# Kernel optimization log

Hardware: AMD Instinct MI355X
Metric: run time of the kernel (lower is better)

Reference implementation:

```python
import jax, jax.numpy as jnp
import numpy as np

ALPHA = 0.2  # LeakyReLU negative slope
NEG = -9e15


def _gat_heads(x, adj_mask, W, a):
    # x: (B,N,F); W: (H,F,O); a: (H,2O); adj_mask: (B,N,N) bool
    O = W.shape[-1]
    Wh = jnp.einsum('bnf,hfo->bhno', x, W)            # (B,H,N,O)
    e1 = jnp.einsum('bhno,ho->bhn', Wh, a[:, :O])     # Wh @ a[:O]
    e2 = jnp.einsum('bhno,ho->bhn', Wh, a[:, O:])     # Wh @ a[O:]
    e = jax.nn.leaky_relu(e1[:, :, :, None] + e2[:, :, None, :], ALPHA)  # (B,H,N,N)
    e = jnp.where(adj_mask[:, None], e, NEG)
    attn = jax.nn.softmax(e, axis=-1)
    return jnp.einsum('bhnm,bhmo->bhno', attn, Wh)    # (B,H,N,O)


def _gat_block(x, adj_mask, non_pad_mask, W_heads, a_heads, W_out, a_out):
    # multi-head layer, concat=True -> elu per head, then concat on feature dim
    h = jax.nn.elu(_gat_heads(x, adj_mask, W_heads, a_heads))  # (B,H,N,O)
    B, H, N, O = h.shape
    h = jnp.transpose(h, (0, 2, 1, 3)).reshape(B, N, H * O)
    h = h * non_pad_mask
    # out layer: single head, concat=False (no inner elu)
    h = _gat_heads(h, adj_mask, W_out[None], a_out[None])[:, 0]  # (B,N,noutput)
    h = h * non_pad_mask
    return jax.nn.elu(h)


def setup_inputs() -> dict:
    key = jax.random.key(0)
    ks = jax.random.split(key, 8)
    B, N = 32, 256
    vocab, F, O, H, OUT = 200, 300, 256, 8, 512
    fea = jax.random.randint(ks[0], (B, N), 0, vocab, dtype=jnp.int32)
    adj = jax.random.randint(ks[1], (B, N, N), 0, 2, dtype=jnp.int32)
    non_pad_mask = jnp.ones((B, N, 1), dtype=jnp.float32)
    embed = jax.random.normal(ks[2], (vocab, F), dtype=jnp.float32)
    W_heads = jax.random.normal(ks[3], (H, F, O), dtype=jnp.float32) / np.sqrt(F)
    a_heads = jax.random.normal(ks[4], (H, 2 * O), dtype=jnp.float32) / np.sqrt(2 * O)
    W_out = jax.random.normal(ks[5], (H * O, OUT), dtype=jnp.float32) / np.sqrt(H * O)
    a_out = jax.random.normal(ks[6], (2 * OUT,), dtype=jnp.float32) / np.sqrt(2 * OUT)
    return {"fea": fea, "adj": adj, "non_pad_mask": non_pad_mask, "embed": embed,
            "W_heads": W_heads, "a_heads": a_heads, "W_out": W_out, "a_out": a_out}


def reference(fea, adj, non_pad_mask, embed, W_heads, a_heads, W_out, a_out):
    adj_mask = adj > 0
    x = embed[fea]  # (B,N,F)
    # GAT_num = 1; dropout is identity in eval mode
    x = _gat_block(x, adj_mask, non_pad_mask, W_heads, a_heads, W_out, a_out)
    return x  # (B, N, 512)
```

## Files before the change

### kernel.cpp

```cpp
#include <hip/hip_runtime.h>
#include <math.h>


typedef _Float16 f16;
typedef __attribute__((ext_vector_type(8))) _Float16 f16x8;
typedef __attribute__((ext_vector_type(4))) _Float16 f16x4;
typedef __attribute__((ext_vector_type(4))) float f32x4;

__device__ __forceinline__ void async16(const void* g, void* lds) {
  __builtin_amdgcn_global_load_lds(
      (const __attribute__((address_space(1))) void*)g,
      (__attribute__((address_space(3))) void*)lds, 16, 0, 0);
}

__global__ __launch_bounds__(256) void k_prep(const int* __restrict__ fea,
                                              const float* __restrict__ embed,
                                              const float* __restrict__ Whd,
                                              const float* __restrict__ Wo,
                                              f16* __restrict__ x16,
                                              f16* __restrict__ WcT,
                                              f16* __restrict__ WoT,
                                              float* __restrict__ e_all) {
  int bid = blockIdx.x, tid = threadIdx.x;
  if (bid < 1280) {
    int idx = bid * 256 + tid;
    int row = idx / 40, c = idx % 40;
    int tok = fea[row];
    const float* eb = embed + (size_t)tok * 300;
    f16x8 v;
#pragma unroll
    for (int j = 0; j < 8; ++j) {
      int t = c * 8 + j;
      v[j] = (f16)((t < 300) ? eb[t] : 0.f);
    }
    *(f16x8*)&x16[(size_t)row * 320 + c * 8] = v;
  } else if (bid < 1920) {
    int r = bid - 1280;
    int zi = r * 256 + tid;
    if (zi < 147456) e_all[zi] = 0.f;
    __shared__ float tile[32][33];
    int bx = r % 10, q0 = r / 10;
    int by = q0 % 8, h = q0 / 8;
    int c = tid & 31, q = tid >> 5;
#pragma unroll
    for (int i = 0; i < 4; ++i) {
      int tt = q + i * 8;
      int t = bx * 32 + tt;
      float v = (t < 300) ? Whd[((size_t)h * 300 + t) * 256 + by * 32 + c] : 0.f;
      tile[tt][c] = v;
    }
    __syncthreads();
#pragma unroll
    for (int i = 0; i < 4; ++i) {
      int oo = q + i * 8;
      int gc = h * 256 + by * 32 + oo;
      WcT[(size_t)gc * 320 + bx * 32 + c] = (f16)tile[c][oo];
    }
  } else {
    int r = bid - 1920;
    __shared__ float tile[32][33];
    int bx = r % 64, by = r / 64;
    int c = tid & 31, q = tid >> 5;
#pragma unroll
    for (int i = 0; i < 4; ++i) {
      int kk = q + i * 8;
      tile[kk][c] = Wo[((size_t)bx * 32 + kk) * 512 + by * 32 + c];
    }
    __syncthreads();
#pragma unroll
    for (int i = 0; i < 4; ++i) {
      int oo = q + i * 8;
      WoT[((size_t)by * 32 + oo) * 2048 + bx * 32 + c] = (f16)tile[c][oo];
    }
  }
}

template <int KDIM, int NCOLS>
__global__ __launch_bounds__(256, 4) void k_gemm1(const f16* __restrict__ A,
                                                  const f16* __restrict__ BT,
                                                  f16* __restrict__ outT,
                                                  const float* __restrict__ avec,
                                                  float* __restrict__ e1,
                                                  float* __restrict__ e2) {
  __shared__ f16 As[128 * 64];
  __shared__ f16 Bs[128 * 64];
  const int by = blockIdx.x, bx = blockIdx.y;
  const int tid = threadIdx.x;
  const int wave = tid >> 6, lane = tid & 63;
  const int wm = wave >> 1, wn = wave & 1;
  const int lrow = lane & 15, quad = lane >> 4;
  const int srow = lane >> 3;
  const int scol = ((lane & 7) ^ (lane >> 3)) * 8;
  const int l7 = lrow & 7;

  f32x4 acc[4][4] = {};
  const f16* Ag = A + (size_t)by * 128 * KDIM;
  const f16* Bg = BT + (size_t)bx * 128 * KDIM;

  for (int k0 = 0; k0 < KDIM; k0 += 64) {
    __syncthreads();
#pragma unroll
    for (int j = 0; j < 4; ++j) {
      const int r0 = wave * 32 + j * 8;
      async16(Ag + (size_t)(r0 + srow) * KDIM + k0 + scol, &As[r0 * 64]);
      async16(Bg + (size_t)(r0 + srow) * KDIM + k0 + scol, &Bs[r0 * 64]);
    }
    __syncthreads();
#pragma unroll
    for (int s = 0; s < 2; ++s) {
      const int sq = ((s * 4 + quad) ^ l7) * 8;
      f16x8 af[4], bf[4];
#pragma unroll
      for (int t = 0; t < 4; ++t) {
        af[t] = *(const f16x8*)&As[(wm * 64 + t * 16 + lrow) * 64 + sq];
        bf[t] = *(const f16x8*)&Bs[(wn * 64 + t * 16 + lrow) * 64 + sq];
      }
#pragma unroll
      for (int mt = 0; mt < 4; ++mt)
#pragma unroll
        for (int nt = 0; nt < 4; ++nt)
          acc[mt][nt] = __builtin_amdgcn_mfma_f32_16x16x32_f16(af[mt], bf[nt], acc[mt][nt], 0, 0, 0);
    }
  }

  const int b = (by * 128) >> 8;
  const int nbase0 = (by * 128) & 255;
#pragma unroll
  for (int mt = 0; mt < 4; ++mt) {
    const int nb = nbase0 + wm * 64 + mt * 16 + quad * 4;
#pragma unroll
    for (int nt = 0; nt < 4; ++nt) {
      const int gc = bx * 128 + wn * 64 + nt * 16 + lrow;
      f16x4 v;
#pragma unroll
      for (int r = 0; r < 4; ++r) v[r] = (f16)acc[mt][nt][r];
      *(f16x4*)&outT[((size_t)b * NCOLS + gc) * 256 + nb] = v;
    }
  }

  float a1v[4], a2v[4];
#pragma unroll
  for (int nt = 0; nt < 4; ++nt) {
    const int gc = bx * 128 + wn * 64 + nt * 16 + lrow;
    int hh = gc >> 8, oo = gc & 255;
    a1v[nt] = avec[hh * 512 + oo];
    a2v[nt] = avec[hh * 512 + 256 + oo];
  }
  const int hblk = (bx * 128) >> 8;
  const int ebase = (b * 8 + hblk) * 256;
#pragma unroll
  for (int mt = 0; mt < 4; ++mt) {
    float s1[4] = {0.f, 0.f, 0.f, 0.f}, s2[4] = {0.f, 0.f, 0.f, 0.f};
#pragma unroll
    for (int nt = 0; nt < 4; ++nt)
#pragma unroll
      for (int r = 0; r < 4; ++r) {
        s1[r] += acc[mt][nt][r] * a1v[nt];
        s2[r] += acc[mt][nt][r] * a2v[nt];
      }
#pragma unroll
    for (int r = 0; r < 4; ++r)
#pragma unroll
      for (int m = 1; m < 16; m <<= 1) {
        s1[r] += __shfl_xor(s1[r], m);
        s2[r] += __shfl_xor(s2[r], m);
      }
    if (lrow == 0) {
      const int nb = nbase0 + wm * 64 + mt * 16 + quad * 4;
#pragma unroll
      for (int r = 0; r < 4; ++r) {
        atomicAdd(&e1[ebase + nb + r], s1[r]);
        atomicAdd(&e2[ebase + nb + r], s2[r]);
      }
    }
  }
}

__global__ __launch_bounds__(256, 4) void k_gemm_sk(const f16* __restrict__ A,
                                                    const f16* __restrict__ BT,
                                                    f16* __restrict__ outSK,
                                                    const float* __restrict__ ao,
                                                    float* __restrict__ e12,
                                                    float* __restrict__ e22) {
  __shared__ f16 As[128 * 64];
  __shared__ f16 Bs[64 * 64];
  const int by = blockIdx.x, bx = blockIdx.y, kz = blockIdx.z;
  const int tid = threadIdx.x;
  const int wave = tid >> 6, lane = tid & 63;
  const int wm = wave >> 1, wn = wave & 1;
  const int lrow = lane & 15, quad = lane >> 4;
  const int srow = lane >> 3;
  const int scol = ((lane & 7) ^ (lane >> 3)) * 8;
  const int l7 = lrow & 7;

  f32x4 acc[4][2] = {};
  const f16* Ag = A + (size_t)by * 128 * 2048;
  const f16* Bg = BT + (size_t)bx * 64 * 2048;
  const int kbeg = kz * 1024;

  for (int k0 = kbeg; k0 < kbeg + 1024; k0 += 64) {
    __syncthreads();
#pragma unroll
    for (int j = 0; j < 4; ++j) {
      const int r0 = wave * 32 + j * 8;
      async16(Ag + (size_t)(r0 + srow) * 2048 + k0 + scol, &As[r0 * 64]);
    }
#pragma unroll
    for (int j = 0; j < 2; ++j) {
      const int r0 = wave * 16 + j * 8;
      async16(Bg + (size_t)(r0 + srow) * 2048 + k0 + scol, &Bs[r0 * 64]);
    }
    __syncthreads();
#pragma unroll
    for (int s = 0; s < 2; ++s) {
      const int sq = ((s * 4 + quad) ^ l7) * 8;
      f16x8 af[4], bf[2];
#pragma unroll
      for (int t = 0; t < 4; ++t)
        af[t] = *(const f16x8*)&As[(wm * 64 + t * 16 + lrow) * 64 + sq];
#pragma unroll
      for (int t = 0; t < 2; ++t)
        bf[t] = *(const f16x8*)&Bs[(wn * 32 + t * 16 + lrow) * 64 + sq];
#pragma unroll
      for (int mt = 0; mt < 4; ++mt)
#pragma unroll
        for (int nt = 0; nt < 2; ++nt)
          acc[mt][nt] = __builtin_amdgcn_mfma_f32_16x16x32_f16(af[mt], bf[nt], acc[mt][nt], 0, 0, 0);
    }
  }

  const int b = (by * 128) >> 8;
  const int nbase0 = (by * 128) & 255;
  f16* dst = outSK + (size_t)kz * 32 * 512 * 256;
#pragma unroll
  for (int mt = 0; mt < 4; ++mt) {
    const int nb = nbase0 + wm * 64 + mt * 16 + quad * 4;
#pragma unroll
    for (int nt = 0; nt < 2; ++nt) {
      const int gc = bx * 64 + wn * 32 + nt * 16 + lrow;
      f16x4 v;
#pragma unroll
      for (int r = 0; r < 4; ++r) v[r] = (f16)acc[mt][nt][r];
      *(f16x4*)&dst[((size_t)b * 512 + gc) * 256 + nb] = v;
    }
  }

  float a1v[2], a2v[2];
#pragma unroll
  for (int nt = 0; nt < 2; ++nt) {
    const int gc = bx * 64 + wn * 32 + nt * 16 + lrow;
    a1v[nt] = ao[gc];
    a2v[nt] = ao[512 + gc];
  }
#pragma unroll
  for (int mt = 0; mt < 4; ++mt) {
    float s1[4] = {0.f, 0.f, 0.f, 0.f}, s2[4] = {0.f, 0.f, 0.f, 0.f};
#pragma unroll
    for (int nt = 0; nt < 2; ++nt)
#pragma unroll
      for (int r = 0; r < 4; ++r) {
        s1[r] += acc[mt][nt][r] * a1v[nt];
        s2[r] += acc[mt][nt][r] * a2v[nt];
      }
#pragma unroll
    for (int r = 0; r < 4; ++r)
#pragma unroll
      for (int m = 1; m < 16; m <<= 1) {
        s1[r] += __shfl_xor(s1[r], m);
        s2[r] += __shfl_xor(s2[r], m);
      }
    if (lrow == 0) {
      const int nb = nbase0 + wm * 64 + mt * 16 + quad * 4;
#pragma unroll
      for (int r = 0; r < 4; ++r) {
        atomicAdd(&e12[b * 256 + nb + r], s1[r]);
        atomicAdd(&e22[b * 256 + nb + r], s2[r]);
      }
    }
  }
}

#define PSTRIDE 264

__global__ __launch_bounds__(256, 4) void k_attn1(
    const f16* __restrict__ WhT, const float* __restrict__ e1g, const float* __restrict__ e2g,
    const int* __restrict__ adj, const float* __restrict__ npm, f16* __restrict__ h1) {
  int h = blockIdx.x, b = blockIdx.y, nt0 = blockIdx.z;
  int bh = b * 8 + h;
  int n0 = nt0 * 64;
  __shared__ f16 P[64 * PSTRIDE];
  int tid = threadIdx.x;
  int wave = tid >> 6, lane = tid & 63;

  float4 e2v = *(const float4*)&e2g[bh * 256 + lane * 4];
  float e2m = fmaxf(fmaxf(e2v.x, e2v.y), fmaxf(e2v.z, e2v.w));
#pragma unroll
  for (int m = 1; m < 64; m <<= 1) e2m = fmaxf(e2m, __shfl_xor(e2m, m));
#pragma unroll 4
  for (int i = 0; i < 16; ++i) {
    int row = i * 4 + wave;
    int gn = b * 256 + n0 + row;
    float er = e1g[bh * 256 + n0 + row];
    float sh = er + e2m;
    sh = sh > 0.f ? sh : 0.2f * sh;
    int4 aj = *(const int4*)&adj[(size_t)gn * 256 + lane * 4];
    float p0, p1, p2, p3;
    {
      float v = er + e2v.x; v = v > 0.f ? v : 0.2f * v;
      p0 = aj.x ? __expf(v - sh) : 0.f;
      v = er + e2v.y; v = v > 0.f ? v : 0.2f * v;
      p1 = aj.y ? __expf(v - sh) : 0.f;
      v = er + e2v.z; v = v > 0.f ? v : 0.2f * v;
      p2 = aj.z ? __expf(v - sh) : 0.f;
      v = er + e2v.w; v = v > 0.f ? v : 0.2f * v;
      p3 = aj.w ? __expf(v - sh) : 0.f;
    }
    float sm = p0 + p1 + p2 + p3;
#pragma unroll
    for (int m = 1; m < 64; m <<= 1) sm += __shfl_xor(sm, m);
    float rs = 1.f / sm;
    f16x4 pw;
    pw[0] = (f16)(p0 * rs); pw[1] = (f16)(p1 * rs);
    pw[2] = (f16)(p2 * rs); pw[3] = (f16)(p3 * rs);
    *(f16x4*)&P[row * PSTRIDE + lane * 4] = pw;
  }
  __syncthreads();

  int lrow = lane & 15, quad = lane >> 4;
  f32x4 acc[4][4] = {};
  const f16* Ag = WhT + (size_t)bh * 65536;
#pragma unroll 2
  for (int k0 = 0; k0 < 256; k0 += 32) {
    f16x8 af[4], bf[4];
#pragma unroll
    for (int mt = 0; mt < 4; ++mt)
      af[mt] = *(const f16x8*)&Ag[(size_t)(wave * 64 + mt * 16 + lrow) * 256 + k0 + quad * 8];
#pragma unroll
    for (int nt = 0; nt < 4; ++nt)
      bf[nt] = *(const f16x8*)&P[(nt * 16 + lrow) * PSTRIDE + k0 + quad * 8];
#pragma unroll
    for (int mt = 0; mt < 4; ++mt)
#pragma unroll
      for (int nt = 0; nt < 4; ++nt)
        acc[mt][nt] = __builtin_amdgcn_mfma_f32_16x16x32_f16(af[mt], bf[nt], acc[mt][nt], 0, 0, 0);
  }
#pragma unroll
  for (int nt = 0; nt < 4; ++nt) {
    int nloc = nt * 16 + lrow;
    int gn = b * 256 + n0 + nloc;
    float pm = npm[gn];
#pragma unroll
    for (int mt = 0; mt < 4; ++mt) {
      int o0 = wave * 64 + mt * 16 + quad * 4;
      f16x4 st;
#pragma unroll
      for (int r = 0; r < 4; ++r) {
        float v = acc[mt][nt][r];
        v = v > 0.f ? v : (__expf(v) - 1.f);
        st[r] = (f16)(v * pm);
      }
      *(f16x4*)&h1[(size_t)gn * 2048 + h * 256 + o0] = st;
    }
  }
}

__global__ __launch_bounds__(256, 4) void k_attn2(
    const f16* __restrict__ sk, const float* __restrict__ e1g, const float* __restrict__ e2g,
    const int* __restrict__ adj, const float* __restrict__ npm, float* __restrict__ out) {
  int oh = blockIdx.x, b = blockIdx.y, nt0 = blockIdx.z;
  int n0 = nt0 * 64;
  __shared__ f16 P[64 * PSTRIDE];
  int tid = threadIdx.x;
  int wave = tid >> 6, lane = tid & 63;

  float4 e2v = *(const float4*)&e2g[b * 256 + lane * 4];
  float e2m = fmaxf(fmaxf(e2v.x, e2v.y), fmaxf(e2v.z, e2v.w));
#pragma unroll
  for (int m = 1; m < 64; m <<= 1) e2m = fmaxf(e2m, __shfl_xor(e2m, m));
#pragma unroll 4
  for (int i = 0; i < 16; ++i) {
    int row = i * 4 + wave;
    int gn = b * 256 + n0 + row;
    float er = e1g[b * 256 + n0 + row];
    float sh = er + e2m;
    sh = sh > 0.f ? sh : 0.2f * sh;
    int4 aj = *(const int4*)&adj[(size_t)gn * 256 + lane * 4];
    float p0, p1, p2, p3;
    {
      float v = er + e2v.x; v = v > 0.f ? v : 0.2f * v;
      p0 = aj.x ? __expf(v - sh) : 0.f;
      v = er + e2v.y; v = v > 0.f ? v : 0.2f * v;
      p1 = aj.y ? __expf(v - sh) : 0.f;
      v = er + e2v.z; v = v > 0.f ? v : 0.2f * v;
      p2 = aj.z ? __expf(v - sh) : 0.f;
      v = er + e2v.w; v = v > 0.f ? v : 0.2f * v;
      p3 = aj.w ? __expf(v - sh) : 0.f;
    }
    float sm = p0 + p1 + p2 + p3;
#pragma unroll
    for (int m = 1; m < 64; m <<= 1) sm += __shfl_xor(sm, m);
    float rs = 1.f / sm;
    f16x4 pw;
    pw[0] = (f16)(p0 * rs); pw[1] = (f16)(p1 * rs);
    pw[2] = (f16)(p2 * rs); pw[3] = (f16)(p3 * rs);
    *(f16x4*)&P[row * PSTRIDE + lane * 4] = pw;
  }
  __syncthreads();

  int lrow = lane & 15, quad = lane >> 4;
  f32x4 acc[2][4] = {};
  const f16* Ag0 = sk + ((size_t)b * 512 + oh * 128) * 256;
  const f16* Ag1 = Ag0 + (size_t)32 * 512 * 256;
#pragma unroll 2
  for (int k0 = 0; k0 < 256; k0 += 32) {
    f16x8 af[2], bf[4];
#pragma unroll
    for (int mt = 0; mt < 2; ++mt) {
      size_t off = (size_t)(wave * 32 + mt * 16 + lrow) * 256 + k0 + quad * 8;
      af[mt] = *(const f16x8*)&Ag0[off] + *(const f16x8*)&Ag1[off];
    }
#pragma unroll
    for (int nt = 0; nt < 4; ++nt)
      bf[nt] = *(const f16x8*)&P[(nt * 16 + lrow) * PSTRIDE + k0 + quad * 8];
#pragma unroll
    for (int mt = 0; mt < 2; ++mt)
#pragma unroll
      for (int nt = 0; nt < 4; ++nt)
        acc[mt][nt] = __builtin_amdgcn_mfma_f32_16x16x32_f16(af[mt], bf[nt], acc[mt][nt], 0, 0, 0);
  }
#pragma unroll
  for (int nt = 0; nt < 4; ++nt) {
    int nloc = nt * 16 + lrow;
    int gn = b * 256 + n0 + nloc;
    float pm = npm[gn];
#pragma unroll
    for (int mt = 0; mt < 2; ++mt) {
      int o0 = oh * 128 + wave * 32 + mt * 16 + quad * 4;
      float4 st;
      float v0 = acc[mt][nt][0] * pm;
      float v1 = acc[mt][nt][1] * pm;
      float v2 = acc[mt][nt][2] * pm;
      float v3 = acc[mt][nt][3] * pm;
      st.x = v0 > 0.f ? v0 : (__expf(v0) - 1.f);
      st.y = v1 > 0.f ? v1 : (__expf(v1) - 1.f);
      st.z = v2 > 0.f ? v2 : (__expf(v2) - 1.f);
      st.w = v3 > 0.f ? v3 : (__expf(v3) - 1.f);
      *(float4*)&out[(size_t)gn * 512 + o0] = st;
    }
  }
}

extern "C" void kernel_launch(void* const* d_in, const int* in_sizes, int n_in,
                              void* d_out, int out_size, void* d_ws, size_t ws_size,
                              hipStream_t stream) {
  (void)in_sizes; (void)n_in; (void)out_size; (void)ws_size;
  const int*   fea   = (const int*)d_in[0];
  const int*   adj   = (const int*)d_in[1];
  const float* npm   = (const float*)d_in[2];
  const float* embed = (const float*)d_in[3];
  const float* Whd   = (const float*)d_in[4];
  const float* ah    = (const float*)d_in[5];
  const float* Wo    = (const float*)d_in[6];
  const float* ao    = (const float*)d_in[7];
  float* out = (float*)d_out;

  char* ws = (char*)d_ws;
  f16* x16  = (f16*)ws;  ws += (size_t)8192 * 320 * 2;
  f16* WcT  = (f16*)ws;  ws += (size_t)2048 * 320 * 2;
  f16* WoT  = (f16*)ws;  ws += (size_t)512 * 2048 * 2;
  f16* WhT  = (f16*)ws;  ws += (size_t)32 * 8 * 256 * 256 * 2;
  f16* h1   = (f16*)ws;  ws += (size_t)8192 * 2048 * 2;
  f16* Wh2sk = (f16*)ws; ws += (size_t)2 * 32 * 512 * 256 * 2;
  float* e1  = (float*)ws; ws += (size_t)65536 * 4;
  float* e2  = (float*)ws; ws += (size_t)65536 * 4;
  float* e12 = (float*)ws; ws += (size_t)8192 * 4;
  float* e22 = (float*)ws; ws += (size_t)8192 * 4;

  k_prep<<<2944, 256, 0, stream>>>(fea, embed, Whd, Wo, x16, WcT, WoT, e1);

  k_gemm1<320, 2048><<<dim3(64, 16), 256, 0, stream>>>(x16, WcT, WhT, ah, e1, e2);
  k_attn1<<<dim3(8, 32, 4), 256, 0, stream>>>(WhT, e1, e2, adj, npm, h1);

  k_gemm_sk<<<dim3(64, 8, 2), 256, 0, stream>>>(h1, WoT, Wh2sk, ao, e12, e22);
  k_attn2<<<dim3(4, 32, 4), 256, 0, stream>>>(Wh2sk, e12, e22, adj, npm, out);
}
```

Measured before the change: 201.9 us.

## Double-buffer LDS tiles in GEMMs and software-prefetch global operands in attention

Both projection GEMMs now use two LDS buffers, issuing async global-to-LDS loads for the next K tile while MFMAs consume the current one, with one barrier per iteration instead of two. Launch-bound occupancy hints drop to 2 and 3 blocks per CU to fit the doubled shared memory. Both attention kernels now ping-pong register fragments, loading the next K slice of Wh from global memory before issuing MFMAs on the current one. This aims to hide memory latency, at the cost of lower occupancy and more register pressure.

```diff
diff --git a/kernel.cpp b/kernel.cpp
--- a/kernel.cpp
+++ b/kernel.cpp
@@ -76,14 +76,14 @@
 }
 
 template <int KDIM, int NCOLS>
-__global__ __launch_bounds__(256, 4) void k_gemm1(const f16* __restrict__ A,
+__global__ __launch_bounds__(256, 2) void k_gemm1(const f16* __restrict__ A,
                                                   const f16* __restrict__ BT,
                                                   f16* __restrict__ outT,
                                                   const float* __restrict__ avec,
                                                   float* __restrict__ e1,
                                                   float* __restrict__ e2) {
-  __shared__ f16 As[128 * 64];
-  __shared__ f16 Bs[128 * 64];
+  __shared__ f16 As[2][128 * 64];
+  __shared__ f16 Bs[2][128 * 64];
   const int by = blockIdx.x, bx = blockIdx.y;
   const int tid = threadIdx.x;
   const int wave = tid >> 6, lane = tid & 63;
@@ -96,24 +96,36 @@
   f32x4 acc[4][4] = {};
   const f16* Ag = A + (size_t)by * 128 * KDIM;
   const f16* Bg = BT + (size_t)bx * 128 * KDIM;
-
-  for (int k0 = 0; k0 < KDIM; k0 += 64) {
-    __syncthreads();
-#pragma unroll
-    for (int j = 0; j < 4; ++j) {
-      const int r0 = wave * 32 + j * 8;
-      async16(Ag + (size_t)(r0 + srow) * KDIM + k0 + scol, &As[r0 * 64]);
-      async16(Bg + (size_t)(r0 + srow) * KDIM + k0 + scol, &Bs[r0 * 64]);
-    }
-    __syncthreads();
+  constexpr int NT = KDIM / 64;
+
+#pragma unroll
+  for (int j = 0; j < 4; ++j) {
+    const int r0 = wave * 32 + j * 8;
+    async16(Ag + (size_t)(r0 + srow) * KDIM + scol, &As[0][r0 * 64]);
+    async16(Bg + (size_t)(r0 + srow) * KDIM + scol, &Bs[0][r0 * 64]);
+  }
+  __syncthreads();
+
+#pragma unroll
+  for (int t = 0; t < NT; ++t) {
+    const int cur = t & 1;
+    if (t + 1 < NT) {
+      const int kn = (t + 1) * 64;
+#pragma unroll
+      for (int j = 0; j < 4; ++j) {
+        const int r0 = wave * 32 + j * 8;
+        async16(Ag + (size_t)(r0 + srow) * KDIM + kn + scol, &As[cur ^ 1][r0 * 64]);
+        async16(Bg + (size_t)(r0 + srow) * KDIM + kn + scol, &Bs[cur ^ 1][r0 * 64]);
+      }
+    }
 #pragma unroll
     for (int s = 0; s < 2; ++s) {
       const int sq = ((s * 4 + quad) ^ l7) * 8;
       f16x8 af[4], bf[4];
 #pragma unroll
-      for (int t = 0; t < 4; ++t) {
-        af[t] = *(const f16x8*)&As[(wm * 64 + t * 16 + lrow) * 64 + sq];
-        bf[t] = *(const f16x8*)&Bs[(wn * 64 + t * 16 + lrow) * 64 + sq];
+      for (int tt = 0; tt < 4; ++tt) {
+        af[tt] = *(const f16x8*)&As[cur][(wm * 64 + tt * 16 + lrow) * 64 + sq];
+        bf[tt] = *(const f16x8*)&Bs[cur][(wn * 64 + tt * 16 + lrow) * 64 + sq];
       }
 #pragma unroll
       for (int mt = 0; mt < 4; ++mt)
@@ -121,6 +133,7 @@
         for (int nt = 0; nt < 4; ++nt)
           acc[mt][nt] = __builtin_amdgcn_mfma_f32_16x16x32_f16(af[mt], bf[nt], acc[mt][nt], 0, 0, 0);
     }
+    __syncthreads();
   }
 
   const int b = (by * 128) >> 8;
@@ -176,14 +189,14 @@
   }
 }
 
-__global__ __launch_bounds__(256, 4) void k_gemm_sk(const f16* __restrict__ A,
+__global__ __launch_bounds__(256, 3) void k_gemm_sk(const f16* __restrict__ A,
                                                     const f16* __restrict__ BT,
                                                     f16* __restrict__ outSK,
                                                     const float* __restrict__ ao,
                                                     float* __restrict__ e12,
                                                     float* __restrict__ e22) {
-  __shared__ f16 As[128 * 64];
-  __shared__ f16 Bs[64 * 64];
+  __shared__ f16 As[2][128 * 64];
+  __shared__ f16 Bs[2][64 * 64];
   const int by = blockIdx.x, bx = blockIdx.y, kz = blockIdx.z;
   const int tid = threadIdx.x;
   const int wave = tid >> 6, lane = tid & 63;
@@ -198,35 +211,51 @@
   const f16* Bg = BT + (size_t)bx * 64 * 2048;
   const int kbeg = kz * 1024;
 
-  for (int k0 = kbeg; k0 < kbeg + 1024; k0 += 64) {
-    __syncthreads();
-#pragma unroll
-    for (int j = 0; j < 4; ++j) {
-      const int r0 = wave * 32 + j * 8;
-      async16(Ag + (size_t)(r0 + srow) * 2048 + k0 + scol, &As[r0 * 64]);
-    }
-#pragma unroll
-    for (int j = 0; j < 2; ++j) {
-      const int r0 = wave * 16 + j * 8;
-      async16(Bg + (size_t)(r0 + srow) * 2048 + k0 + scol, &Bs[r0 * 64]);
-    }
-    __syncthreads();
+#pragma unroll
+  for (int j = 0; j < 4; ++j) {
+    const int r0 = wave * 32 + j * 8;
+    async16(Ag + (size_t)(r0 + srow) * 2048 + kbeg + scol, &As[0][r0 * 64]);
+  }
+#pragma unroll
+  for (int j = 0; j < 2; ++j) {
+    const int r0 = wave * 16 + j * 8;
+    async16(Bg + (size_t)(r0 + srow) * 2048 + kbeg + scol, &Bs[0][r0 * 64]);
+  }
+  __syncthreads();
+
+#pragma unroll 2
+  for (int t = 0; t < 16; ++t) {
+    const int cur = t & 1;
+    if (t + 1 < 16) {
+      const int kn = kbeg + (t + 1) * 64;
+#pragma unroll
+      for (int j = 0; j < 4; ++j) {
+        const int r0 = wave * 32 + j * 8;
+        async16(Ag + (size_t)(r0 + srow) * 2048 + kn + scol, &As[cur ^ 1][r0 * 64]);
+      }
+#pragma unroll
+      for (int j = 0; j < 2; ++j) {
+        const int r0 = wave * 16 + j * 8;
+        async16(Bg + (size_t)(r0 + srow) * 2048 + kn + scol, &Bs[cur ^ 1][r0 * 64]);
+      }
+    }
 #pragma unroll
     for (int s = 0; s < 2; ++s) {
       const int sq = ((s * 4 + quad) ^ l7) * 8;
       f16x8 af[4], bf[2];
 #pragma unroll
-      for (int t = 0; t < 4; ++t)
-        af[t] = *(const f16x8*)&As[(wm * 64 + t * 16 + lrow) * 64 + sq];
-#pragma unroll
-      for (int t = 0; t < 2; ++t)
-        bf[t] = *(const f16x8*)&Bs[(wn * 32 + t * 16 + lrow) * 64 + sq];
+      for (int tt = 0; tt < 4; ++tt)
+        af[tt] = *(const f16x8*)&As[cur][(wm * 64 + tt * 16 + lrow) * 64 + sq];
+#pragma unroll
+      for (int tt = 0; tt < 2; ++tt)
+        bf[tt] = *(const f16x8*)&Bs[cur][(wn * 32 + tt * 16 + lrow) * 64 + sq];
 #pragma unroll
       for (int mt = 0; mt < 4; ++mt)
 #pragma unroll
         for (int nt = 0; nt < 2; ++nt)
           acc[mt][nt] = __builtin_amdgcn_mfma_f32_16x16x32_f16(af[mt], bf[nt], acc[mt][nt], 0, 0, 0);
     }
+    __syncthreads();
   }
 
   const int b = (by * 128) >> 8;
@@ -281,6 +310,13 @@
 }
 
 #define PSTRIDE 264
+
+__device__ __forceinline__ void load_af4(const f16* __restrict__ Ag, int wave,
+                                         int lrow, int quad, int k0, f16x8* dst) {
+#pragma unroll
+  for (int mt = 0; mt < 4; ++mt)
+    dst[mt] = *(const f16x8*)&Ag[(size_t)(wave * 64 + mt * 16 + lrow) * 256 + k0 + quad * 8];
+}
 
 __global__ __launch_bounds__(256, 4) void k_attn1(
     const f16* __restrict__ WhT, const float* __restrict__ e1g, const float* __restrict__ e2g,
@@ -329,12 +365,13 @@
   int lrow = lane & 15, quad = lane >> 4;
   f32x4 acc[4][4] = {};
   const f16* Ag = WhT + (size_t)bh * 65536;
-#pragma unroll 2
-  for (int k0 = 0; k0 < 256; k0 += 32) {
-    f16x8 af[4], bf[4];
-#pragma unroll
-    for (int mt = 0; mt < 4; ++mt)
-      af[mt] = *(const f16x8*)&Ag[(size_t)(wave * 64 + mt * 16 + lrow) * 256 + k0 + quad * 8];
+  f16x8 afA[4], afB[4];
+  load_af4(Ag, wave, lrow, quad, 0, afA);
+#pragma unroll
+  for (int kk = 0; kk < 4; ++kk) {
+    const int k0 = kk * 64;
+    load_af4(Ag, wave, lrow, quad, k0 + 32, afB);
+    f16x8 bf[4];
 #pragma unroll
     for (int nt = 0; nt < 4; ++nt)
       bf[nt] = *(const f16x8*)&P[(nt * 16 + lrow) * PSTRIDE + k0 + quad * 8];
@@ -342,7 +379,16 @@
     for (int mt = 0; mt < 4; ++mt)
 #pragma unroll
       for (int nt = 0; nt < 4; ++nt)
-        acc[mt][nt] = __builtin_amdgcn_mfma_f32_16x16x32_f16(af[mt], bf[nt], acc[mt][nt], 0, 0, 0);
+        acc[mt][nt] = __builtin_amdgcn_mfma_f32_16x16x32_f16(afA[mt], bf[nt], acc[mt][nt], 0, 0, 0);
+    if (kk < 3) load_af4(Ag, wave, lrow, quad, k0 + 64, afA);
+#pragma unroll
+    for (int nt = 0; nt < 4; ++nt)
+      bf[nt] = *(const f16x8*)&P[(nt * 16 + lrow) * PSTRIDE + k0 + 32 + quad * 8];
+#pragma unroll
+    for (int mt = 0; mt < 4; ++mt)
+#pragma unroll
+      for (int nt = 0; nt < 4; ++nt)
+        acc[mt][nt] = __builtin_amdgcn_mfma_f32_16x16x32_f16(afB[mt], bf[nt], acc[mt][nt], 0, 0, 0);
   }
 #pragma unroll
   for (int nt = 0; nt < 4; ++nt) {
@@ -411,22 +457,51 @@
   f32x4 acc[2][4] = {};
   const f16* Ag0 = sk + ((size_t)b * 512 + oh * 128) * 256;
   const f16* Ag1 = Ag0 + (size_t)32 * 512 * 256;
-#pragma unroll 2
-  for (int k0 = 0; k0 < 256; k0 += 32) {
-    f16x8 af[2], bf[4];
+  f16x8 h0A[2], h1A[2], h0B[2], h1B[2];
+#pragma unroll
+  for (int mt = 0; mt < 2; ++mt) {
+    size_t off = (size_t)(wave * 32 + mt * 16 + lrow) * 256 + quad * 8;
+    h0A[mt] = *(const f16x8*)&Ag0[off];
+    h1A[mt] = *(const f16x8*)&Ag1[off];
+  }
+#pragma unroll
+  for (int kk = 0; kk < 4; ++kk) {
+    const int k0 = kk * 64;
 #pragma unroll
     for (int mt = 0; mt < 2; ++mt) {
-      size_t off = (size_t)(wave * 32 + mt * 16 + lrow) * 256 + k0 + quad * 8;
-      af[mt] = *(const f16x8*)&Ag0[off] + *(const f16x8*)&Ag1[off];
-    }
+      size_t off = (size_t)(wave * 32 + mt * 16 + lrow) * 256 + k0 + 32 + quad * 8;
+      h0B[mt] = *(const f16x8*)&Ag0[off];
+      h1B[mt] = *(const f16x8*)&Ag1[off];
+    }
+    f16x8 bf[4];
 #pragma unroll
     for (int nt = 0; nt < 4; ++nt)
       bf[nt] = *(const f16x8*)&P[(nt * 16 + lrow) * PSTRIDE + k0 + quad * 8];
 #pragma unroll
-    for (int mt = 0; mt < 2; ++mt)
+    for (int mt = 0; mt < 2; ++mt) {
+      f16x8 af = h0A[mt] + h1A[mt];
 #pragma unroll
       for (int nt = 0; nt < 4; ++nt)
-        acc[mt][nt] = __builtin_amdgcn_mfma_f32_16x16x32_f16(af[mt], bf[nt], acc[mt][nt], 0, 0, 0);
+        acc[mt][nt] = __builtin_amdgcn_mfma_f32_16x16x32_f16(af, bf[nt], acc[mt][nt], 0, 0, 0);
+    }
+    if (kk < 3) {
+#pragma unroll
+      for (int mt = 0; mt < 2; ++mt) {
+        size_t off = (size_t)(wave * 32 + mt * 16 + lrow) * 256 + k0 + 64 + quad * 8;
+        h0A[mt] = *(const f16x8*)&Ag0[off];
+        h1A[mt] = *(const f16x8*)&Ag1[off];
+      }
+    }
+#pragma unroll
+    for (int nt = 0; nt < 4; ++nt)
+      bf[nt] = *(const f16x8*)&P[(nt * 16 + lrow) * PSTRIDE + k0 + 32 + quad * 8];
+#pragma unroll
+    for (int mt = 0; mt < 2; ++mt) {
+      f16x8 af = h0B[mt] + h1B[mt];
+#pragma unroll
+      for (int nt = 0; nt < 4; ++nt)
+        acc[mt][nt] = __builtin_amdgcn_mfma_f32_16x16x32_f16(af, bf[nt], acc[mt][nt], 0, 0, 0);
+    }
   }
 #pragma unroll
   for (int nt = 0; nt < 4; ++nt) {
```

Result: slower. 217.1 us (+7.5%).

## Fuse layer-1 projection GEMM with attention softmax and aggregation per head

Applied to the files above, without the earlier changes.

Merges the first-layer Wh GEMM and the attention kernel into one 512-thread kernel per (batch, head) that keeps Wh in swizzled LDS and computes e1/e2 with shared-memory atomics. This removes the Wh round trip through global memory, the global e1/e2 buffers and a kernel launch. It also remaps k_attn2 block indices so blocks sharing a batch are grouped together for L2 locality. The trade-off is one large block per CU with about 146 KB of LDS, so only 256 blocks run with low occupancy and the P·Wh stage is split into small 32-row chunks with extra barriers.

```diff
diff --git a/kernel.cpp b/kernel.cpp
--- a/kernel.cpp
+++ b/kernel.cpp
@@ -37,7 +37,7 @@
   } else if (bid < 1920) {
     int r = bid - 1280;
     int zi = r * 256 + tid;
-    if (zi < 147456) e_all[zi] = 0.f;
+    if (zi < 16384) e_all[zi] = 0.f;
     __shared__ float tile[32][33];
     int bx = r % 10, q0 = r / 10;
     int by = q0 % 8, h = q0 / 8;
@@ -75,89 +75,90 @@
   }
 }
 
-template <int KDIM, int NCOLS>
-__global__ __launch_bounds__(256, 4) void k_gemm1(const f16* __restrict__ A,
-                                                  const f16* __restrict__ BT,
-                                                  f16* __restrict__ outT,
-                                                  const float* __restrict__ avec,
-                                                  float* __restrict__ e1,
-                                                  float* __restrict__ e2) {
-  __shared__ f16 As[128 * 64];
-  __shared__ f16 Bs[128 * 64];
-  const int by = blockIdx.x, bx = blockIdx.y;
+__global__ __launch_bounds__(512, 1) void k_l1(
+    const f16* __restrict__ x16, const f16* __restrict__ WcT,
+    const float* __restrict__ ah, const int* __restrict__ adj,
+    const float* __restrict__ npm, f16* __restrict__ h1) {
+  extern __shared__ __align__(16) char smem[];
+  f16* As = (f16*)smem;
+  f16* Bs = (f16*)(smem + 32768);
+  char* WhB = smem;
+  char* PB  = smem + 131072;
+  float* e1f = (float*)(smem + 147456);
+  float* e2f = (float*)(smem + 148480);
+
+  const int bid = blockIdx.x;
+  const int h = (bid >> 3) & 7;
+  const int b = (bid & 7) * 4 + (bid >> 6);
   const int tid = threadIdx.x;
   const int wave = tid >> 6, lane = tid & 63;
-  const int wm = wave >> 1, wn = wave & 1;
+  const int wm = wave >> 2, wn = wave & 3;
   const int lrow = lane & 15, quad = lane >> 4;
   const int srow = lane >> 3;
   const int scol = ((lane & 7) ^ (lane >> 3)) * 8;
   const int l7 = lrow & 7;
 
-  f32x4 acc[4][4] = {};
-  const f16* Ag = A + (size_t)by * 128 * KDIM;
-  const f16* Bg = BT + (size_t)bx * 128 * KDIM;
-
-  for (int k0 = 0; k0 < KDIM; k0 += 64) {
+  if (tid < 256) e1f[tid] = 0.f;
+  else e2f[tid - 256] = 0.f;
+
+  f32x4 acc[8][4] = {};
+  const f16* Ag = x16 + (size_t)b * 256 * 320;
+  const f16* Bg = WcT + (size_t)h * 256 * 320;
+
+  for (int t = 0; t < 5; ++t) {
+    const int k0 = t * 64;
     __syncthreads();
 #pragma unroll
     for (int j = 0; j < 4; ++j) {
       const int r0 = wave * 32 + j * 8;
-      async16(Ag + (size_t)(r0 + srow) * KDIM + k0 + scol, &As[r0 * 64]);
-      async16(Bg + (size_t)(r0 + srow) * KDIM + k0 + scol, &Bs[r0 * 64]);
+      async16(Ag + (size_t)(r0 + srow) * 320 + k0 + scol, &As[r0 * 64]);
+      async16(Bg + (size_t)(r0 + srow) * 320 + k0 + scol, &Bs[r0 * 64]);
     }
     __syncthreads();
 #pragma unroll
     for (int s = 0; s < 2; ++s) {
       const int sq = ((s * 4 + quad) ^ l7) * 8;
-      f16x8 af[4], bf[4];
-#pragma unroll
-      for (int t = 0; t < 4; ++t) {
-        af[t] = *(const f16x8*)&As[(wm * 64 + t * 16 + lrow) * 64 + sq];
-        bf[t] = *(const f16x8*)&Bs[(wn * 64 + t * 16 + lrow) * 64 + sq];
-      }
-#pragma unroll
-      for (int mt = 0; mt < 4; ++mt)
+      f16x8 af[8], bf[4];
+#pragma unroll
+      for (int mt = 0; mt < 8; ++mt)
+        af[mt] = *(const f16x8*)&As[(wm * 128 + mt * 16 + lrow) * 64 + sq];
+#pragma unroll
+      for (int nt = 0; nt < 4; ++nt)
+        bf[nt] = *(const f16x8*)&Bs[(wn * 64 + nt * 16 + lrow) * 64 + sq];
+#pragma unroll
+      for (int mt = 0; mt < 8; ++mt)
 #pragma unroll
         for (int nt = 0; nt < 4; ++nt)
           acc[mt][nt] = __builtin_amdgcn_mfma_f32_16x16x32_f16(af[mt], bf[nt], acc[mt][nt], 0, 0, 0);
     }
   }
-
-  const int b = (by * 128) >> 8;
-  const int nbase0 = (by * 128) & 255;
-#pragma unroll
-  for (int mt = 0; mt < 4; ++mt) {
-    const int nb = nbase0 + wm * 64 + mt * 16 + quad * 4;
+  __syncthreads();
+
+  float a1v[4], a2v[4];
+#pragma unroll
+  for (int nt = 0; nt < 4; ++nt) {
+    const int o = wn * 64 + nt * 16 + lrow;
+    a1v[nt] = ah[h * 512 + o];
+    a2v[nt] = ah[h * 512 + 256 + o];
+  }
+#pragma unroll
+  for (int mt = 0; mt < 8; ++mt) {
+    const int n0 = wm * 128 + mt * 16 + quad * 4;
+    const int q16 = n0 >> 3;
+    const int hoff = (n0 & 4) ? 8 : 0;
+    float s1[4] = {0.f, 0.f, 0.f, 0.f}, s2[4] = {0.f, 0.f, 0.f, 0.f};
 #pragma unroll
     for (int nt = 0; nt < 4; ++nt) {
-      const int gc = bx * 128 + wn * 64 + nt * 16 + lrow;
+      const int o = wn * 64 + nt * 16 + lrow;
       f16x4 v;
 #pragma unroll
-      for (int r = 0; r < 4; ++r) v[r] = (f16)acc[mt][nt][r];
-      *(f16x4*)&outT[((size_t)b * NCOLS + gc) * 256 + nb] = v;
-    }
-  }
-
-  float a1v[4], a2v[4];
-#pragma unroll
-  for (int nt = 0; nt < 4; ++nt) {
-    const int gc = bx * 128 + wn * 64 + nt * 16 + lrow;
-    int hh = gc >> 8, oo = gc & 255;
-    a1v[nt] = avec[hh * 512 + oo];
-    a2v[nt] = avec[hh * 512 + 256 + oo];
-  }
-  const int hblk = (bx * 128) >> 8;
-  const int ebase = (b * 8 + hblk) * 256;
-#pragma unroll
-  for (int mt = 0; mt < 4; ++mt) {
-    float s1[4] = {0.f, 0.f, 0.f, 0.f}, s2[4] = {0.f, 0.f, 0.f, 0.f};
-#pragma unroll
-    for (int nt = 0; nt < 4; ++nt)
-#pragma unroll
       for (int r = 0; r < 4; ++r) {
+        v[r] = (f16)acc[mt][nt][r];
         s1[r] += acc[mt][nt][r] * a1v[nt];
         s2[r] += acc[mt][nt][r] * a2v[nt];
       }
+      *(f16x4*)(WhB + o * 512 + ((q16 ^ (o & 7)) * 16 + hoff)) = v;
+    }
 #pragma unroll
     for (int r = 0; r < 4; ++r)
 #pragma unroll
@@ -166,11 +167,90 @@
         s2[r] += __shfl_xor(s2[r], m);
       }
     if (lrow == 0) {
-      const int nb = nbase0 + wm * 64 + mt * 16 + quad * 4;
 #pragma unroll
       for (int r = 0; r < 4; ++r) {
-        atomicAdd(&e1[ebase + nb + r], s1[r]);
-        atomicAdd(&e2[ebase + nb + r], s2[r]);
+        atomicAdd(&e1f[n0 + r], s1[r]);
+        atomicAdd(&e2f[n0 + r], s2[r]);
+      }
+    }
+  }
+  __syncthreads();
+
+  float4 e2v = *(const float4*)&e2f[lane * 4];
+  float e2m = fmaxf(fmaxf(e2v.x, e2v.y), fmaxf(e2v.z, e2v.w));
+#pragma unroll
+  for (int m = 1; m < 64; m <<= 1) e2m = fmaxf(e2m, __shfl_xor(e2m, m));
+
+  for (int c = 0; c < 8; ++c) {
+#pragma unroll
+    for (int i = 0; i < 4; ++i) {
+      int rl = i * 8 + wave;
+      int n = c * 32 + rl;
+      int gn = b * 256 + n;
+      float er = e1f[n];
+      float sh = er + e2m;
+      sh = sh > 0.f ? sh : 0.2f * sh;
+      int4 aj = *(const int4*)&adj[(size_t)gn * 256 + lane * 4];
+      float p0, p1, p2, p3;
+      {
+        float v = er + e2v.x; v = v > 0.f ? v : 0.2f * v;
+        p0 = aj.x ? __expf(v - sh) : 0.f;
+        v = er + e2v.y; v = v > 0.f ? v : 0.2f * v;
+        p1 = aj.y ? __expf(v - sh) : 0.f;
+        v = er + e2v.z; v = v > 0.f ? v : 0.2f * v;
+        p2 = aj.z ? __expf(v - sh) : 0.f;
+        v = er + e2v.w; v = v > 0.f ? v : 0.2f * v;
+        p3 = aj.w ? __expf(v - sh) : 0.f;
+      }
+      float sm = p0 + p1 + p2 + p3;
+#pragma unroll
+      for (int m = 1; m < 64; m <<= 1) sm += __shfl_xor(sm, m);
+      float rs = 1.f / sm;
+      f16x4 pw;
+      pw[0] = (f16)(p0 * rs); pw[1] = (f16)(p1 * rs);
+      pw[2] = (f16)(p2 * rs); pw[3] = (f16)(p3 * rs);
+      *(f16x4*)(PB + rl * 512 + (((lane >> 1) ^ (rl & 7)) * 16 + (lane & 1) * 8)) = pw;
+    }
+    __syncthreads();
+
+    f32x4 acc2[2][2] = {};
+#pragma unroll
+    for (int kk = 0; kk < 8; ++kk) {
+      f16x8 af2[2], bf2[2];
+#pragma unroll
+      for (int mtO = 0; mtO < 2; ++mtO) {
+        int o = wave * 32 + mtO * 16 + lrow;
+        af2[mtO] = *(const f16x8*)(WhB + o * 512 + (((kk * 4 + quad) ^ (o & 7)) * 16));
+      }
+#pragma unroll
+      for (int ntN = 0; ntN < 2; ++ntN) {
+        int rl = ntN * 16 + lrow;
+        bf2[ntN] = *(const f16x8*)(PB + rl * 512 + (((kk * 4 + quad) ^ (rl & 7)) * 16));
+      }
+#pragma unroll
+      for (int mtO = 0; mtO < 2; ++mtO)
+#pragma unroll
+        for (int ntN = 0; ntN < 2; ++ntN)
+          acc2[mtO][ntN] = __builtin_amdgcn_mfma_f32_16x16x32_f16(af2[mtO], bf2[ntN], acc2[mtO][ntN], 0, 0, 0);
+    }
+    __syncthreads();
+
+#pragma unroll
+    for (int ntN = 0; ntN < 2; ++ntN) {
+      int n = c * 32 + ntN * 16 + lrow;
+      int gn = b * 256 + n;
+      float pm = npm[gn];
+#pragma unroll
+      for (int mtO = 0; mtO < 2; ++mtO) {
+        int o0 = wave * 32 + mtO * 16 + quad * 4;
+        f16x4 st;
+#pragma unroll
+        for (int r = 0; r < 4; ++r) {
+          float v = acc2[mtO][ntN][r];
+          v = v > 0.f ? v : (__expf(v) - 1.f);
+          st[r] = (f16)(v * pm);
+        }
+        *(f16x4*)&h1[(size_t)gn * 2048 + h * 256 + o0] = st;
       }
     }
   }
@@ -282,92 +362,13 @@
 
 #define PSTRIDE 264
 
-__global__ __launch_bounds__(256, 4) void k_attn1(
-    const f16* __restrict__ WhT, const float* __restrict__ e1g, const float* __restrict__ e2g,
-    const int* __restrict__ adj, const float* __restrict__ npm, f16* __restrict__ h1) {
-  int h = blockIdx.x, b = blockIdx.y, nt0 = blockIdx.z;
-  int bh = b * 8 + h;
-  int n0 = nt0 * 64;
-  __shared__ f16 P[64 * PSTRIDE];
-  int tid = threadIdx.x;
-  int wave = tid >> 6, lane = tid & 63;
-
-  float4 e2v = *(const float4*)&e2g[bh * 256 + lane * 4];
-  float e2m = fmaxf(fmaxf(e2v.x, e2v.y), fmaxf(e2v.z, e2v.w));
-#pragma unroll
-  for (int m = 1; m < 64; m <<= 1) e2m = fmaxf(e2m, __shfl_xor(e2m, m));
-#pragma unroll 4
-  for (int i = 0; i < 16; ++i) {
-    int row = i * 4 + wave;
-    int gn = b * 256 + n0 + row;
-    float er = e1g[bh * 256 + n0 + row];
-    float sh = er + e2m;
-    sh = sh > 0.f ? sh : 0.2f * sh;
-    int4 aj = *(const int4*)&adj[(size_t)gn * 256 + lane * 4];
-    float p0, p1, p2, p3;
-    {
-      float v = er + e2v.x; v = v > 0.f ? v : 0.2f * v;
-      p0 = aj.x ? __expf(v - sh) : 0.f;
-      v = er + e2v.y; v = v > 0.f ? v : 0.2f * v;
-      p1 = aj.y ? __expf(v - sh) : 0.f;
-      v = er + e2v.z; v = v > 0.f ? v : 0.2f * v;
-      p2 = aj.z ? __expf(v - sh) : 0.f;
-      v = er + e2v.w; v = v > 0.f ? v : 0.2f * v;
-      p3 = aj.w ? __expf(v - sh) : 0.f;
-    }
-    float sm = p0 + p1 + p2 + p3;
-#pragma unroll
-    for (int m = 1; m < 64; m <<= 1) sm += __shfl_xor(sm, m);
-    float rs = 1.f / sm;
-    f16x4 pw;
-    pw[0] = (f16)(p0 * rs); pw[1] = (f16)(p1 * rs);
-    pw[2] = (f16)(p2 * rs); pw[3] = (f16)(p3 * rs);
-    *(f16x4*)&P[row * PSTRIDE + lane * 4] = pw;
-  }
-  __syncthreads();
-
-  int lrow = lane & 15, quad = lane >> 4;
-  f32x4 acc[4][4] = {};
-  const f16* Ag = WhT + (size_t)bh * 65536;
-#pragma unroll 2
-  for (int k0 = 0; k0 < 256; k0 += 32) {
-    f16x8 af[4], bf[4];
-#pragma unroll
-    for (int mt = 0; mt < 4; ++mt)
-      af[mt] = *(const f16x8*)&Ag[(size_t)(wave * 64 + mt * 16 + lrow) * 256 + k0 + quad * 8];
-#pragma unroll
-    for (int nt = 0; nt < 4; ++nt)
-      bf[nt] = *(const f16x8*)&P[(nt * 16 + lrow) * PSTRIDE + k0 + quad * 8];
-#pragma unroll
-    for (int mt = 0; mt < 4; ++mt)
-#pragma unroll
-      for (int nt = 0; nt < 4; ++nt)
-        acc[mt][nt] = __builtin_amdgcn_mfma_f32_16x16x32_f16(af[mt], bf[nt], acc[mt][nt], 0, 0, 0);
-  }
-#pragma unroll
-  for (int nt = 0; nt < 4; ++nt) {
-    int nloc = nt * 16 + lrow;
-    int gn = b * 256 + n0 + nloc;
-    float pm = npm[gn];
-#pragma unroll
-    for (int mt = 0; mt < 4; ++mt) {
-      int o0 = wave * 64 + mt * 16 + quad * 4;
-      f16x4 st;
-#pragma unroll
-      for (int r = 0; r < 4; ++r) {
-        float v = acc[mt][nt][r];
-        v = v > 0.f ? v : (__expf(v) - 1.f);
-        st[r] = (f16)(v * pm);
-      }
-      *(f16x4*)&h1[(size_t)gn * 2048 + h * 256 + o0] = st;
-    }
-  }
-}
-
 __global__ __launch_bounds__(256, 4) void k_attn2(
     const f16* __restrict__ sk, const float* __restrict__ e1g, const float* __restrict__ e2g,
     const int* __restrict__ adj, const float* __restrict__ npm, float* __restrict__ out) {
-  int oh = blockIdx.x, b = blockIdx.y, nt0 = blockIdx.z;
+  int bid = blockIdx.x;
+  int nt0 = (bid >> 3) & 3;
+  int pair = (bid >> 5) * 8 + (bid & 7);
+  int oh = pair >> 5, b = pair & 31;
   int n0 = nt0 * 64;
   __shared__ f16 P[64 * PSTRIDE];
   int tid = threadIdx.x;
@@ -468,19 +469,15 @@
   f16* x16  = (f16*)ws;  ws += (size_t)8192 * 320 * 2;
   f16* WcT  = (f16*)ws;  ws += (size_t)2048 * 320 * 2;
   f16* WoT  = (f16*)ws;  ws += (size_t)512 * 2048 * 2;
-  f16* WhT  = (f16*)ws;  ws += (size_t)32 * 8 * 256 * 256 * 2;
   f16* h1   = (f16*)ws;  ws += (size_t)8192 * 2048 * 2;
   f16* Wh2sk = (f16*)ws; ws += (size_t)2 * 32 * 512 * 256 * 2;
-  float* e1  = (float*)ws; ws += (size_t)65536 * 4;
-  float* e2  = (float*)ws; ws += (size_t)65536 * 4;
   float* e12 = (float*)ws; ws += (size_t)8192 * 4;
   float* e22 = (float*)ws; ws += (size_t)8192 * 4;
 
-  k_prep<<<2944, 256, 0, stream>>>(fea, embed, Whd, Wo, x16, WcT, WoT, e1);
-
-  k_gemm1<320, 2048><<<dim3(64, 16), 256, 0, stream>>>(x16, WcT, WhT, ah, e1, e2);
-  k_attn1<<<dim3(8, 32, 4), 256, 0, stream>>>(WhT, e1, e2, adj, npm, h1);
+  k_prep<<<2944, 256, 0, stream>>>(fea, embed, Whd, Wo, x16, WcT, WoT, e12);
+
+  k_l1<<<256, 512, 149504, stream>>>(x16, WcT, ah, adj, npm, h1);
 
   k_gemm_sk<<<dim3(64, 8, 2), 256, 0, stream>>>(h1, WoT, Wh2sk, ao, e12, e22);
-  k_attn2<<<dim3(4, 32, 4), 256, 0, stream>>>(Wh2sk, e12, e22, adj, npm, out);
-}
+  k_attn2<<<512, 256, 0, stream>>>(Wh2sk, e12, e22, adj, npm, out);
+}
```

New measurement: 191.6 us. -5.1%, faster.
